# Kernel tuning notes

Measured on AMD Instinct MI355X. Metric: run time of the kernel, lower is better.

## Reference

```python
import jax, jax.numpy as jnp
import numpy as np
from functools import partial

ALPHA = 2.0  # ATan surrogate alpha (spikingjelly default)
V_TH = 1.0   # v_threshold

@jax.custom_vjp
def atan_spike(x):
    # heaviside(x) with ATan surrogate gradient
    return (x >= 0.0).astype(x.dtype)

def _atan_fwd(x):
    return atan_spike(x), x

def _atan_bwd(x, g):
    # d/dx [1/pi * atan(pi/2 * alpha * x) + 1/2] = (alpha/2) / (1 + (pi/2*alpha*x)^2)
    pi_half_alpha = jnp.asarray(np.pi / 2.0 * ALPHA, x.dtype)
    sg = (ALPHA / 2.0) / (1.0 + (pi_half_alpha * x) ** 2)
    return (g * sg,)

atan_spike.defvjp(_atan_fwd, _atan_bwd)

def plif(x_seq, w):
    """ParametricLIFNode, step_mode='m', hard reset to v_reset=0, detach_reset=True.
    x_seq: [T, B, C, H, W].  H_t = V_{t-1} + (X_t - V_{t-1}) * sigmoid(w)."""
    decay = jax.nn.sigmoid(w)
    def step(v, x):
        h = v + (x - v) * decay
        s = atan_spike(h - V_TH)
        v_next = (1.0 - jax.lax.stop_gradient(s)) * h  # hard reset to 0, detached
        return v_next, s
    _, s_seq = jax.lax.scan(step, jnp.zeros_like(x_seq[0]), x_seq)
    return s_seq

def conv1x1(x, w, b):
    # x: [T,B,C,H,W], w: [O,C], b: [O] -> [T,B,O,H,W]
    y = jnp.einsum('tbchw,oc->tbohw', x, w)
    return y + b[None, None, :, None, None]

def setup_inputs() -> dict:
    key = jax.random.key(0)
    ks = jax.random.split(key, 3)
    T, B, C, H, W = 4, 32, 384, 14, 14
    hid = 1536
    x = jax.random.normal(ks[0], (T, B, C, H, W), dtype=jnp.float32)
    # kaiming-ish init scaled by fan-in
    w1 = jax.random.normal(ks[1], (hid, C), dtype=jnp.float32) / np.sqrt(C)
    b1 = jnp.zeros((hid,), dtype=jnp.float32)
    w2 = jax.random.normal(ks[2], (C, hid), dtype=jnp.float32) / np.sqrt(hid)
    b2 = jnp.zeros((C,), dtype=jnp.float32)
    pw1 = jnp.zeros((), dtype=jnp.float32)  # init_tau=2 -> w=-log(tau-1)=0
    pw2 = jnp.zeros((), dtype=jnp.float32)
    return {"x": x, "pw1": pw1, "w1": w1, "b1": b1, "pw2": pw2, "w2": w2, "b2": b2}

def reference(x, pw1, w1, b1, pw2, w2, b2):
    # CMlp.forward: act1 -> fc1 -> (drop=0) -> act2 -> fc2 -> (drop=0)
    s1 = plif(x, pw1)
    h = conv1x1(s1, w1, b1)
    s2 = plif(h, pw2)
    out = conv1x1(s2, w2, b2)
    return out
```

## Files before the change

### kernel.cpp

```cpp
#include <hip/hip_runtime.h>
#include <hip/hip_bf16.h>
#include <cstdint>

#define T_   4
#define B_   32
#define C_   384
#define HID  1536
#define P_   196
#define MTOT 25088

using f32x4  = __attribute__((ext_vector_type(4))) float;
using bf16x8 = __attribute__((ext_vector_type(8))) __bf16;

static __device__ __forceinline__ unsigned short f32_to_bf16(float f) {
  unsigned int u = __builtin_bit_cast(unsigned int, f);
  unsigned int r = (u + 0x7FFFu + ((u >> 16) & 1u)) >> 16;
  return (unsigned short)r;
}
static __device__ __forceinline__ float bf16_to_f32(unsigned short h) {
  return __builtin_bit_cast(float, ((unsigned int)h) << 16);
}

static __device__ __forceinline__ f32x4 mfma16x16x32(bf16x8 a, bf16x8 b, f32x4 c) {
  return __builtin_amdgcn_mfma_f32_16x16x32_bf16(a, b, c, 0, 0, 0);
}

#define GLDS(src, dst)                                                              \
  __builtin_amdgcn_global_load_lds((const __attribute__((address_space(1))) void*)(src), \
                                   (__attribute__((address_space(3))) void*)(dst), 16, 0, 0)

__global__ __launch_bounds__(256) void prep_w(const float* __restrict__ w1, const float* __restrict__ w2,
                                              unsigned short* __restrict__ w1h, unsigned short* __restrict__ w1l,
                                              unsigned short* __restrict__ w2h, unsigned short* __restrict__ w2l) {
  int i = blockIdx.x * 256 + threadIdx.x;
  if (i >= C_ * HID) return;
  float a = w1[i];
  unsigned short h = f32_to_bf16(a);
  w1h[i] = h;
  w1l[i] = f32_to_bf16(a - bf16_to_f32(h));
  float b = w2[i];
  unsigned short h2 = f32_to_bf16(b);
  w2h[i] = h2;
  w2l[i] = f32_to_bf16(b - bf16_to_f32(h2));
}

__global__ __launch_bounds__(256) void plif1_t(const float* __restrict__ x, const float* __restrict__ pw1,
                                               unsigned short* __restrict__ s1t) {
  __shared__ float xt[64][65];
  int b = blockIdx.x, c0 = blockIdx.y * 64, p0 = blockIdx.z * 64;
  int tid  = threadIdx.x;
  int c    = tid & 63;
  int prow = tid >> 6;
  float d1 = 1.0f / (1.0f + expf(-pw1[0]));
  float v[16];
#pragma unroll
  for (int k = 0; k < 16; ++k) v[k] = 0.0f;

  for (int t = 0; t < 4; ++t) {
    __syncthreads();
#pragma unroll
    for (int i = 0; i < 16; ++i) {
      int l = tid + i * 256;
      int cl = l >> 6, pl = l & 63;
      if (p0 + pl < P_)
        xt[cl][pl] = x[(size_t)((t * B_ + b) * C_ + c0 + cl) * P_ + p0 + pl];
    }
    __syncthreads();
#pragma unroll
    for (int k = 0; k < 16; ++k) {
      int p = prow + 4 * k;
      if (p0 + p < P_) {
        float xv = xt[c][p];
        float H  = v[k] + (xv - v[k]) * d1;
        bool  s  = (H - 1.0f) >= 0.0f;
        s1t[(size_t)((b * P_ + p0 + p) * 4 + t) * C_ + c0 + c] = s ? (unsigned short)0x3F80 : (unsigned short)0;
        v[k] = s ? 0.0f : H;
      }
    }
  }
}

__global__ __launch_bounds__(256) void gemm1_plif2(const unsigned short* __restrict__ s1t,
                                                   const unsigned short* __restrict__ w1h,
                                                   const unsigned short* __restrict__ w1l,
                                                   const float* __restrict__ b1, const float* __restrict__ pw2,
                                                   unsigned short* __restrict__ s2) {
  __shared__ unsigned short As[128 * 64];
  __shared__ unsigned short Bh[128 * 64];
  __shared__ unsigned short Bl[128 * 64];
  int tid = threadIdx.x;
  int lane = tid & 63, wave = tid >> 6;
  int wm = wave >> 1, wn = wave & 1;
  int gid = blockIdx.x;
  int xcd = gid & 7, pos = gid >> 3;
  int lin = xcd * 294 + pos;
  int bx = lin / 12, by = lin - bx * 12;
  int m0 = bx * 128, n0 = by * 128;

  f32x4 acc[4][4];
#pragma unroll
  for (int m = 0; m < 4; ++m)
#pragma unroll
    for (int n = 0; n < 4; ++n) acc[m][n] = (f32x4)0.0f;

  for (int kt = 0; kt < C_ / 64; ++kt) {
    int k0 = kt * 64;
#pragma unroll
    for (int i = 0; i < 4; ++i) {
      int l = i * 256 + tid;
      int row = l >> 3;
      int kblk = (l & 7) ^ (row & 7);
      const unsigned short* sA = s1t + (size_t)(m0 + row) * C_ + k0 + kblk * 8;
      const unsigned short* sH = w1h + (size_t)(n0 + row) * C_ + k0 + kblk * 8;
      const unsigned short* sL = w1l + (size_t)(n0 + row) * C_ + k0 + kblk * 8;
      unsigned short* dA = As + i * 2048 + wave * 512;
      unsigned short* dH = Bh + i * 2048 + wave * 512;
      unsigned short* dL = Bl + i * 2048 + wave * 512;
      GLDS(sA, dA);
      GLDS(sH, dH);
      GLDS(sL, dL);
    }
    __syncthreads();
#pragma unroll
    for (int ks = 0; ks < 2; ++ks) {
      bf16x8 a[4], bh[4], bl[4];
      int kof = ks * 32 + ((lane >> 4) << 3);
#pragma unroll
      for (int m = 0; m < 4; ++m) {
        int row = wm * 64 + m * 16 + (lane & 15);
        a[m] = *(const bf16x8*)&As[row * 64 + (kof ^ ((row & 7) << 3))];
      }
#pragma unroll
      for (int n = 0; n < 4; ++n) {
        int row = wn * 64 + n * 16 + (lane & 15);
        int idx = row * 64 + (kof ^ ((row & 7) << 3));
        bh[n] = *(const bf16x8*)&Bh[idx];
        bl[n] = *(const bf16x8*)&Bl[idx];
      }
#pragma unroll
      for (int m = 0; m < 4; ++m)
#pragma unroll
        for (int n = 0; n < 4; ++n) {
          acc[m][n] = mfma16x16x32(a[m], bh[n], acc[m][n]);
          acc[m][n] = mfma16x16x32(a[m], bl[n], acc[m][n]);
        }
    }
    __syncthreads();
  }

  float d2 = 1.0f / (1.0f + expf(-pw2[0]));
#pragma unroll
  for (int n = 0; n < 4; ++n) {
    int colg = n0 + wn * 64 + n * 16 + (lane & 15);
    float bias = b1[colg];
#pragma unroll
    for (int m = 0; m < 4; ++m) {
      int rowbase = m0 + wm * 64 + m * 16 + ((lane >> 4) << 2);
      float v = 0.0f;
#pragma unroll
      for (int i = 0; i < 4; ++i) {
        float xv = acc[m][n][i] + bias;
        float H  = v + (xv - v) * d2;
        bool  s  = (H - 1.0f) >= 0.0f;
        s2[(size_t)(rowbase + i) * HID + colg] = s ? (unsigned short)0x3F80 : (unsigned short)0;
        v = s ? 0.0f : H;
      }
    }
  }
}

__global__ __launch_bounds__(256) void gemm2_out(const unsigned short* __restrict__ s2,
                                                 const unsigned short* __restrict__ w2h,
                                                 const unsigned short* __restrict__ w2l,
                                                 const float* __restrict__ b2, float* __restrict__ out) {
  __shared__ unsigned short As[128 * 64];
  __shared__ unsigned short Bh[64 * 64];
  __shared__ unsigned short Bl[64 * 64];
  int tid = threadIdx.x;
  int lane = tid & 63, wave = tid >> 6;
  int wm = wave >> 1, wn = wave & 1;
  int gid = blockIdx.x;
  int xcd = gid & 7, pos = gid >> 3;
  int lin = xcd * 147 + pos;
  int bx = lin / 6, by = lin - bx * 6;
  int m0 = bx * 128, n0 = by * 64;

  f32x4 acc[4][2];
#pragma unroll
  for (int m = 0; m < 4; ++m)
#pragma unroll
    for (int n = 0; n < 2; ++n) acc[m][n] = (f32x4)0.0f;

  for (int kt = 0; kt < HID / 64; ++kt) {
    int k0 = kt * 64;
#pragma unroll
    for (int i = 0; i < 4; ++i) {
      int l = i * 256 + tid;
      int row = l >> 3;
      int kblk = (l & 7) ^ (row & 7);
      const unsigned short* sA = s2 + (size_t)(m0 + row) * HID + k0 + kblk * 8;
      GLDS(sA, As + i * 2048 + wave * 512);
    }
#pragma unroll
    for (int i = 0; i < 2; ++i) {
      int l = i * 256 + tid;
      int row = l >> 3;
      int kblk = (l & 7) ^ (row & 7);
      const unsigned short* sH = w2h + (size_t)(n0 + row) * HID + k0 + kblk * 8;
      const unsigned short* sL = w2l + (size_t)(n0 + row) * HID + k0 + kblk * 8;
      GLDS(sH, Bh + i * 2048 + wave * 512);
      GLDS(sL, Bl + i * 2048 + wave * 512);
    }
    __syncthreads();
#pragma unroll
    for (int ks = 0; ks < 2; ++ks) {
      bf16x8 a[4], bh[2], bl[2];
      int kof = ks * 32 + ((lane >> 4) << 3);
#pragma unroll
      for (int m = 0; m < 4; ++m) {
        int row = wm * 64 + m * 16 + (lane & 15);
        a[m] = *(const bf16x8*)&As[row * 64 + (kof ^ ((row & 7) << 3))];
      }
#pragma unroll
      for (int n = 0; n < 2; ++n) {
        int row = wn * 32 + n * 16 + (lane & 15);
        int idx = row * 64 + (kof ^ ((row & 7) << 3));
        bh[n] = *(const bf16x8*)&Bh[idx];
        bl[n] = *(const bf16x8*)&Bl[idx];
      }
#pragma unroll
      for (int m = 0; m < 4; ++m)
#pragma unroll
        for (int n = 0; n < 2; ++n) {
          acc[m][n] = mfma16x16x32(a[m], bh[n], acc[m][n]);
          acc[m][n] = mfma16x16x32(a[m], bl[n], acc[m][n]);
        }
    }
    __syncthreads();
  }

#pragma unroll
  for (int n = 0; n < 2; ++n) {
    int colg = n0 + wn * 32 + n * 16 + (lane & 15);
    float bias = b2[colg];
#pragma unroll
    for (int m = 0; m < 4; ++m) {
      int rowbase = m0 + wm * 64 + m * 16 + ((lane >> 4) << 2);
      int pix = rowbase >> 2;
      int bb  = pix / P_;
      int p   = pix - bb * P_;
#pragma unroll
      for (int i = 0; i < 4; ++i) {
        out[(size_t)((i * B_ + bb) * C_ + colg) * P_ + p] = acc[m][n][i] + bias;
      }
    }
  }
}

extern "C" void kernel_launch(void* const* d_in, const int* in_sizes, int n_in,
                              void* d_out, int out_size, void* d_ws, size_t ws_size,
                              hipStream_t stream) {
  const float* x   = (const float*)d_in[0];
  const float* pw1 = (const float*)d_in[1];
  const float* w1  = (const float*)d_in[2];
  const float* b1  = (const float*)d_in[3];
  const float* pw2 = (const float*)d_in[4];
  const float* w2  = (const float*)d_in[5];
  const float* b2  = (const float*)d_in[6];
  float* out = (float*)d_out;

  char* ws = (char*)d_ws;
  unsigned short* s1t = (unsigned short*)(ws);
  unsigned short* s2  = (unsigned short*)(ws + 19267584);
  unsigned short* w1h = (unsigned short*)(ws + 19267584 + 77070336);
  unsigned short* w1l = w1h + 589824;
  unsigned short* w2h = w1l + 589824;
  unsigned short* w2l = w2h + 589824;
  (void)in_sizes; (void)n_in; (void)out_size; (void)ws_size;

  prep_w<<<(C_ * HID + 255) / 256, 256, 0, stream>>>(w1, w2, w1h, w1l, w2h, w2l);
  plif1_t<<<dim3(B_, C_ / 64, 4), 256, 0, stream>>>(x, pw1, s1t);
  gemm1_plif2<<<dim3(MTOT / 128 * (HID / 128)), 256, 0, stream>>>(s1t, w1h, w1l, b1, pw2, s2);
  gemm2_out<<<dim3(MTOT / 128 * (C_ / 64)), 256, 0, stream>>>(s2, w2h, w2l, b2, out);
}
```

Baseline: 162.8 us.

## Triple-buffer LDS with async global-to-LDS prefetch in both GEMM kernels

Replaces the single-buffer load/sync/compute loops in both GEMMs with a three-stage ring of LDS buffers holding K=32 slices, prefetched two stages ahead via global_load_lds. Raw s_waitcnt vmcnt and s_barrier replace __syncthreads so compute on one stage overlaps loads of later stages. It also changes the LDS layout to a k-block-major arrangement without the XOR swizzle, and raises MFMA priority with s_setprio. This aims to hide global memory latency. The cost is more LDS, hand-counted waitcnt values that must stay correct, and possible LDS bank conflicts from the unswizzled layout.

Result: slower. 268.3 us (+64.8%).

```diff
diff --git a/kernel.cpp b/kernel.cpp
--- a/kernel.cpp
+++ b/kernel.cpp
@@ -28,6 +28,10 @@
 #define GLDS(src, dst)                                                              \
   __builtin_amdgcn_global_load_lds((const __attribute__((address_space(1))) void*)(src), \
                                    (__attribute__((address_space(3))) void*)(dst), 16, 0, 0)
+
+#define VMW(N)  asm volatile("s_waitcnt vmcnt(" #N ")" ::: "memory")
+#define LG0     asm volatile("s_waitcnt lgkmcnt(0)" ::: "memory")
+#define BARRIER asm volatile("s_barrier" ::: "memory")
 
 __global__ __launch_bounds__(256) void prep_w(const float* __restrict__ w1, const float* __restrict__ w2,
                                               unsigned short* __restrict__ w1h, unsigned short* __restrict__ w1l,
@@ -85,9 +89,9 @@
                                                    const unsigned short* __restrict__ w1l,
                                                    const float* __restrict__ b1, const float* __restrict__ pw2,
                                                    unsigned short* __restrict__ s2) {
-  __shared__ unsigned short As[128 * 64];
-  __shared__ unsigned short Bh[128 * 64];
-  __shared__ unsigned short Bl[128 * 64];
+  __shared__ unsigned short As[3 * 4096];
+  __shared__ unsigned short Bhs[3 * 4096];
+  __shared__ unsigned short Bls[3 * 4096];
   int tid = threadIdx.x;
   int lane = tid & 63, wave = tid >> 6;
   int wm = wave >> 1, wn = wave & 1;
@@ -103,50 +107,50 @@
 #pragma unroll
     for (int n = 0; n < 4; ++n) acc[m][n] = (f32x4)0.0f;
 
-  for (int kt = 0; kt < C_ / 64; ++kt) {
-    int k0 = kt * 64;
-#pragma unroll
-    for (int i = 0; i < 4; ++i) {
-      int l = i * 256 + tid;
-      int row = l >> 3;
-      int kblk = (l & 7) ^ (row & 7);
-      const unsigned short* sA = s1t + (size_t)(m0 + row) * C_ + k0 + kblk * 8;
-      const unsigned short* sH = w1h + (size_t)(n0 + row) * C_ + k0 + kblk * 8;
-      const unsigned short* sL = w1l + (size_t)(n0 + row) * C_ + k0 + kblk * 8;
-      unsigned short* dA = As + i * 2048 + wave * 512;
-      unsigned short* dH = Bh + i * 2048 + wave * 512;
-      unsigned short* dL = Bl + i * 2048 + wave * 512;
-      GLDS(sA, dA);
-      GLDS(sH, dH);
-      GLDS(sL, dL);
-    }
-    __syncthreads();
-#pragma unroll
-    for (int ks = 0; ks < 2; ++ks) {
-      bf16x8 a[4], bh[4], bl[4];
-      int kof = ks * 32 + ((lane >> 4) << 3);
-#pragma unroll
-      for (int m = 0; m < 4; ++m) {
-        int row = wm * 64 + m * 16 + (lane & 15);
-        a[m] = *(const bf16x8*)&As[row * 64 + (kof ^ ((row & 7) << 3))];
-      }
-#pragma unroll
-      for (int n = 0; n < 4; ++n) {
-        int row = wn * 64 + n * 16 + (lane & 15);
-        int idx = row * 64 + (kof ^ ((row & 7) << 3));
-        bh[n] = *(const bf16x8*)&Bh[idx];
-        bl[n] = *(const bf16x8*)&Bl[idx];
-      }
-#pragma unroll
-      for (int m = 0; m < 4; ++m)
-#pragma unroll
-        for (int n = 0; n < 4; ++n) {
-          acc[m][n] = mfma16x16x32(a[m], bh[n], acc[m][n]);
-          acc[m][n] = mfma16x16x32(a[m], bl[n], acc[m][n]);
-        }
-    }
-    __syncthreads();
-  }
+  const int aBase = ((lane >> 4) * 128 + wm * 64 + (lane & 15)) * 8;
+  const int bBase = ((lane >> 4) * 128 + wn * 64 + (lane & 15)) * 8;
+
+#define G1_STAGE(bi, kt) do { int _k0 = (kt) * 32;                                     \
+    _Pragma("unroll") for (int _j = 0; _j < 2; ++_j) {                                 \
+      GLDS(s1t + (size_t)(m0 + _j * 64 + lane) * C_ + _k0 + wave * 8,                  \
+           As  + (bi) * 4096 + wave * 1024 + _j * 512);                                \
+      GLDS(w1h + (size_t)(n0 + _j * 64 + lane) * C_ + _k0 + wave * 8,                  \
+           Bhs + (bi) * 4096 + wave * 1024 + _j * 512);                                \
+      GLDS(w1l + (size_t)(n0 + _j * 64 + lane) * C_ + _k0 + wave * 8,                  \
+           Bls + (bi) * 4096 + wave * 1024 + _j * 512);                                \
+    } } while (0)
+
+#define G1_BODY(bi) do {                                                               \
+    bf16x8 a[4], bh[4], bl[4];                                                         \
+    _Pragma("unroll") for (int m = 0; m < 4; ++m)                                      \
+      a[m] = *(const bf16x8*)(As + (bi) * 4096 + aBase + m * 128);                     \
+    _Pragma("unroll") for (int n = 0; n < 4; ++n) {                                    \
+      bh[n] = *(const bf16x8*)(Bhs + (bi) * 4096 + bBase + n * 128);                   \
+      bl[n] = *(const bf16x8*)(Bls + (bi) * 4096 + bBase + n * 128);                   \
+    }                                                                                  \
+    LG0; BARRIER;                                                                      \
+    __builtin_amdgcn_s_setprio(1);                                                     \
+    _Pragma("unroll") for (int m = 0; m < 4; ++m)                                      \
+      _Pragma("unroll") for (int n = 0; n < 4; ++n) {                                  \
+        acc[m][n] = mfma16x16x32(a[m], bh[n], acc[m][n]);                              \
+        acc[m][n] = mfma16x16x32(a[m], bl[n], acc[m][n]);                              \
+      }                                                                                \
+    __builtin_amdgcn_s_setprio(0);                                                     \
+  } while (0)
+
+  G1_STAGE(0, 0);
+  G1_STAGE(1, 1);
+  int bc = 0, bs = 2;
+  for (int t = 0; t < 10; ++t) {
+    G1_STAGE(bs, t + 2); bs = (bs == 2) ? 0 : bs + 1;
+    VMW(12);
+    BARRIER;
+    G1_BODY(bc); bc = (bc == 2) ? 0 : bc + 1;
+  }
+  VMW(6);  BARRIER; G1_BODY(bc); bc = (bc == 2) ? 0 : bc + 1;
+  VMW(0);  BARRIER; G1_BODY(bc);
+#undef G1_STAGE
+#undef G1_BODY
 
   float d2 = 1.0f / (1.0f + expf(-pw2[0]));
 #pragma unroll
@@ -173,9 +177,9 @@
                                                  const unsigned short* __restrict__ w2h,
                                                  const unsigned short* __restrict__ w2l,
                                                  const float* __restrict__ b2, float* __restrict__ out) {
-  __shared__ unsigned short As[128 * 64];
-  __shared__ unsigned short Bh[64 * 64];
-  __shared__ unsigned short Bl[64 * 64];
+  __shared__ unsigned short As[3 * 4096];
+  __shared__ unsigned short Bhs[3 * 2048];
+  __shared__ unsigned short Bls[3 * 2048];
   int tid = threadIdx.x;
   int lane = tid & 63, wave = tid >> 6;
   int wm = wave >> 1, wn = wave & 1;
@@ -191,53 +195,50 @@
 #pragma unroll
     for (int n = 0; n < 2; ++n) acc[m][n] = (f32x4)0.0f;
 
-  for (int kt = 0; kt < HID / 64; ++kt) {
-    int k0 = kt * 64;
-#pragma unroll
-    for (int i = 0; i < 4; ++i) {
-      int l = i * 256 + tid;
-      int row = l >> 3;
-      int kblk = (l & 7) ^ (row & 7);
-      const unsigned short* sA = s2 + (size_t)(m0 + row) * HID + k0 + kblk * 8;
-      GLDS(sA, As + i * 2048 + wave * 512);
-    }
-#pragma unroll
-    for (int i = 0; i < 2; ++i) {
-      int l = i * 256 + tid;
-      int row = l >> 3;
-      int kblk = (l & 7) ^ (row & 7);
-      const unsigned short* sH = w2h + (size_t)(n0 + row) * HID + k0 + kblk * 8;
-      const unsigned short* sL = w2l + (size_t)(n0 + row) * HID + k0 + kblk * 8;
-      GLDS(sH, Bh + i * 2048 + wave * 512);
-      GLDS(sL, Bl + i * 2048 + wave * 512);
-    }
-    __syncthreads();
-#pragma unroll
-    for (int ks = 0; ks < 2; ++ks) {
-      bf16x8 a[4], bh[2], bl[2];
-      int kof = ks * 32 + ((lane >> 4) << 3);
-#pragma unroll
-      for (int m = 0; m < 4; ++m) {
-        int row = wm * 64 + m * 16 + (lane & 15);
-        a[m] = *(const bf16x8*)&As[row * 64 + (kof ^ ((row & 7) << 3))];
-      }
-#pragma unroll
-      for (int n = 0; n < 2; ++n) {
-        int row = wn * 32 + n * 16 + (lane & 15);
-        int idx = row * 64 + (kof ^ ((row & 7) << 3));
-        bh[n] = *(const bf16x8*)&Bh[idx];
-        bl[n] = *(const bf16x8*)&Bl[idx];
-      }
-#pragma unroll
-      for (int m = 0; m < 4; ++m)
-#pragma unroll
-        for (int n = 0; n < 2; ++n) {
-          acc[m][n] = mfma16x16x32(a[m], bh[n], acc[m][n]);
-          acc[m][n] = mfma16x16x32(a[m], bl[n], acc[m][n]);
-        }
-    }
-    __syncthreads();
-  }
+  const int aBase = ((lane >> 4) * 128 + wm * 64 + (lane & 15)) * 8;
+  const int bBase = ((lane >> 4) * 64 + wn * 32 + (lane & 15)) * 8;
+
+#define G2_STAGE(bi, kt) do { int _k0 = (kt) * 32;                                     \
+    _Pragma("unroll") for (int _j = 0; _j < 2; ++_j)                                   \
+      GLDS(s2 + (size_t)(m0 + _j * 64 + lane) * HID + _k0 + wave * 8,                  \
+           As + (bi) * 4096 + wave * 1024 + _j * 512);                                 \
+    GLDS(w2h + (size_t)(n0 + lane) * HID + _k0 + wave * 8,                             \
+         Bhs + (bi) * 2048 + wave * 512);                                              \
+    GLDS(w2l + (size_t)(n0 + lane) * HID + _k0 + wave * 8,                             \
+         Bls + (bi) * 2048 + wave * 512);                                              \
+  } while (0)
+
+#define G2_BODY(bi) do {                                                               \
+    bf16x8 a[4], bh[2], bl[2];                                                         \
+    _Pragma("unroll") for (int m = 0; m < 4; ++m)                                      \
+      a[m] = *(const bf16x8*)(As + (bi) * 4096 + aBase + m * 128);                     \
+    _Pragma("unroll") for (int n = 0; n < 2; ++n) {                                    \
+      bh[n] = *(const bf16x8*)(Bhs + (bi) * 2048 + bBase + n * 128);                   \
+      bl[n] = *(const bf16x8*)(Bls + (bi) * 2048 + bBase + n * 128);                   \
+    }                                                                                  \
+    LG0; BARRIER;                                                                      \
+    __builtin_amdgcn_s_setprio(1);                                                     \
+    _Pragma("unroll") for (int m = 0; m < 4; ++m)                                      \
+      _Pragma("unroll") for (int n = 0; n < 2; ++n) {                                  \
+        acc[m][n] = mfma16x16x32(a[m], bh[n], acc[m][n]);                              \
+        acc[m][n] = mfma16x16x32(a[m], bl[n], acc[m][n]);                              \
+      }                                                                                \
+    __builtin_amdgcn_s_setprio(0);                                                     \
+  } while (0)
+
+  G2_STAGE(0, 0);
+  G2_STAGE(1, 1);
+  int bc = 0, bs = 2;
+  for (int t = 0; t < 46; ++t) {
+    G2_STAGE(bs, t + 2); bs = (bs == 2) ? 0 : bs + 1;
+    VMW(8);
+    BARRIER;
+    G2_BODY(bc); bc = (bc == 2) ? 0 : bc + 1;
+  }
+  VMW(4);  BARRIER; G2_BODY(bc); bc = (bc == 2) ? 0 : bc + 1;
+  VMW(0);  BARRIER; G2_BODY(bc);
+#undef G2_STAGE
+#undef G2_BODY
 
 #pragma unroll
   for (int n = 0; n < 2; ++n) {
```
